# Performance work log

Hardware: AMD Instinct MI355X
Metric: run time of the kernel (lower is better)

The kernel has to match this reference:

```python
import jax, jax.numpy as jnp
import numpy as np

B, S, DIM, NH = 2, 2048, 1536, 12
HD = DIM // NH            # 128
C = HD // 2               # 64 rotary pairs
CF = C - 2 * (C // 3)     # 22 (frame axis)
CH = C // 3               # 21 (height axis)
CW = C // 3               # 21 (width axis)
GF, GH, GW = 8, 16, 16    # grid sizes, GF*GH*GW == S
EPS = 1e-6


def _freq_table(n_pos, dim):
    inv = 1.0 / (10000.0 ** (np.arange(dim, dtype=np.float64) / dim))
    ang = np.outer(np.arange(n_pos, dtype=np.float64), inv)
    return (np.cos(ang).astype(np.float32), np.sin(ang).astype(np.float32))


def setup_inputs() -> dict:
    key = jax.random.key(0)
    ks = jax.random.split(key, 8)
    scale = 0.02
    cos_f, sin_f = _freq_table(GF, CF)
    cos_h, sin_h = _freq_table(GH, CH)
    cos_w, sin_w = _freq_table(GW, CW)
    return {
        'x': jax.random.normal(ks[0], (B, S, DIM), dtype=jnp.float32),
        'seq_lens': jnp.array([2048, 1600], dtype=jnp.int32),
        'f': GF, 'h': GH, 'w': GW,
        'wq': scale * jax.random.normal(ks[1], (DIM, DIM), dtype=jnp.float32),
        'bq': jnp.zeros((DIM,), jnp.float32),
        'wk': scale * jax.random.normal(ks[2], (DIM, DIM), dtype=jnp.float32),
        'bk': jnp.zeros((DIM,), jnp.float32),
        'wv': scale * jax.random.normal(ks[3], (DIM, DIM), dtype=jnp.float32),
        'bv': jnp.zeros((DIM,), jnp.float32),
        'wo': scale * jax.random.normal(ks[4], (DIM, DIM), dtype=jnp.float32),
        'bo': jnp.zeros((DIM,), jnp.float32),
        'nq_w': jnp.ones((DIM,), jnp.float32),
        'nk_w': jnp.ones((DIM,), jnp.float32),
        'cos_f': jnp.asarray(cos_f), 'sin_f': jnp.asarray(sin_f),
        'cos_h': jnp.asarray(cos_h), 'sin_h': jnp.asarray(sin_h),
        'cos_w': jnp.asarray(cos_w), 'sin_w': jnp.asarray(sin_w),
    }


def _rmsnorm(t, wt):
    return t * jax.lax.rsqrt(jnp.mean(t * t, axis=-1, keepdims=True) + EPS) * wt


def _grid_rope(t, cos, sin, b, s):
    # t: [b, s, NH, HD] ; cos/sin: [s, 1, C] (per-position assembled freqs)
    tp = t.reshape(b, s, NH, C, 2)
    xr, xi = tp[..., 0], tp[..., 1]
    rr = xr * cos - xi * sin          # complex multiply by e^{i*theta}
    ri = xr * sin + xi * cos
    return jnp.stack([rr, ri], axis=-1).reshape(b, s, NH, HD)


def reference(x, seq_lens, f, h, w, wq, bq, wk, bk, wv, bv, wo, bo,
              nq_w, nk_w, cos_f, sin_f, cos_h, sin_h, cos_w, sin_w):
    b, s, _ = x.shape
    # QKV projections with RMSNorm on q/k over full dim (as in the module)
    q = _rmsnorm(x @ wq.T + bq, nq_w).reshape(b, s, NH, HD)
    k = _rmsnorm(x @ wk.T + bk, nk_w).reshape(b, s, NH, HD)
    v = (x @ wv.T + bv).reshape(b, s, NH, HD)
    # grid-indexed RoPE: zero offsets / target==grid => arange sampling per axis
    idx = jnp.arange(s)
    fi = idx // (h * w)
    hi = (idx // w) % h
    wi = idx % w
    cos = jnp.concatenate([cos_f[fi], cos_h[hi], cos_w[wi]], axis=-1)[:, None, :]
    sin = jnp.concatenate([sin_f[fi], sin_h[hi], sin_w[wi]], axis=-1)[:, None, :]
    qr = _grid_rope(q, cos, sin, b, s)
    kr = _grid_rope(k, cos, sin, b, s)
    # attention with ragged key-length masking (flash_attention k_lens)
    scale = 1.0 / jnp.sqrt(jnp.float32(HD))
    scores = jnp.einsum('bqnd,bknd->bnqk', qr, kr) * scale
    kmask = idx[None, :] < seq_lens[:, None]            # [b, s]
    scores = jnp.where(kmask[:, None, None, :], scores, jnp.float32(-1e30))
    attn = jax.nn.softmax(scores, axis=-1)
    out = jnp.einsum('bnqk,bknd->bqnd', attn, v).reshape(b, s, DIM)
    return out @ wo.T + bo
```

## Files before the change

kernel.cpp:

```cpp
#include <hip/hip_runtime.h>
#include <hip/hip_bf16.h>
#include <math.h>

#define DIM_  1536
#define NH_   12
#define HD_   128
#define S_    2048
#define B_    2
#define M_    (B_*S_)

typedef __attribute__((ext_vector_type(8))) _Float16 f16x8;
typedef __attribute__((ext_vector_type(4))) short short4v;
typedef __attribute__((ext_vector_type(8))) short short8v;
typedef __attribute__((ext_vector_type(4))) float f32x4;

#define SSCALE_LOG2E (0.08838834764831845f * 1.4426950408889634f)

static __device__ __forceinline__ short f2h(float f) {
  union { _Float16 h; short s; } u;
  u.h = (_Float16)f;
  return u.s;
}

static __device__ __forceinline__ unsigned pk2h(float a, float b) {
  typedef __attribute__((ext_vector_type(2))) __fp16 fp16x2;
  union { fp16x2 v; unsigned u; } u2;
  u2.v = __builtin_amdgcn_cvt_pkrtz(a, b);
  return u2.u;
}

__global__ __launch_bounds__(256) void f2h_k(
    const float* __restrict__ in, short* __restrict__ out, int n8)
{
  int i = blockIdx.x * 256 + threadIdx.x;
  if (i >= n8) return;
  const float4* p = (const float4*)in + (size_t)i * 2;
  float4 a = p[0], b = p[1];
  short8v o;
  o[0] = f2h(a.x); o[1] = f2h(a.y); o[2] = f2h(a.z); o[3] = f2h(a.w);
  o[4] = f2h(b.x); o[5] = f2h(b.y); o[6] = f2h(b.z); o[7] = f2h(b.w);
  *((short8v*)out + i) = o;
}

static __device__ __forceinline__ void gemm128_core(
    const short* __restrict__ A16, const float* __restrict__ W,
    const float* __restrict__ bias, float* __restrict__ Out,
    int m0, int n0)
{
  __shared__ __align__(16) char Atile[8192];
  __shared__ __align__(16) char Btile[8192];
  const int tid = threadIdx.x;
  const int l  = tid & 63, w = tid >> 6;
  const int wr = w >> 1, wc = w & 1;
  const int lc = l & 15, lg = l >> 4;

  f32x4 acc[4][4] = {};

  for (int k0 = 0; k0 < DIM_; k0 += 32) {
#pragma unroll
    for (int i = 0; i < 2; ++i) {
      int row   = i * 64 + w * 16 + (l >> 2);
      int slot  = l & 3;
      int gslot = slot ^ ((row >> 1) & 3);
      const short* g = A16 + (size_t)(m0 + row) * DIM_ + k0 + gslot * 8;
      __builtin_amdgcn_global_load_lds(
          (const __attribute__((address_space(1))) unsigned*)g,
          (__attribute__((address_space(3))) unsigned*)(Atile + i * 4096 + w * 1024),
          16, 0, 0);
    }
#pragma unroll
    for (int i = 0; i < 4; ++i) {
      int e   = tid + i * 256;
      int row = e >> 3, f4 = e & 7;
      float4 v4 = *(const float4*)(W + (size_t)(n0 + row) * DIM_ + k0 + f4 * 4);
      short4v h4;
      h4[0] = f2h(v4.x); h4[1] = f2h(v4.y); h4[2] = f2h(v4.z); h4[3] = f2h(v4.w);
      int slot = f4 >> 1;
      *(short4v*)(Btile + row * 64 + (((slot ^ ((row >> 1) & 3)) << 4)) + ((f4 & 1) << 3)) = h4;
    }
    __syncthreads();

    f16x8 af[4], bf[4];
#pragma unroll
    for (int mt = 0; mt < 4; ++mt) {
      int ar = wr * 64 + mt * 16 + lc;
      af[mt] = *(const f16x8*)(Atile + ar * 64 + ((lg ^ ((ar >> 1) & 3)) << 4));
    }
#pragma unroll
    for (int nt = 0; nt < 4; ++nt) {
      int br = wc * 64 + nt * 16 + lc;
      bf[nt] = *(const f16x8*)(Btile + br * 64 + ((lg ^ ((br >> 1) & 3)) << 4));
    }
#pragma unroll
    for (int mt = 0; mt < 4; ++mt)
#pragma unroll
      for (int nt = 0; nt < 4; ++nt)
        acc[mt][nt] = __builtin_amdgcn_mfma_f32_16x16x32_f16(af[mt], bf[nt], acc[mt][nt], 0, 0, 0);
    __syncthreads();
  }

#pragma unroll
  for (int nt = 0; nt < 4; ++nt) {
    int col = n0 + wc * 64 + nt * 16 + lc;
    float bb = bias[col];
#pragma unroll
    for (int mt = 0; mt < 4; ++mt) {
#pragma unroll
      for (int r = 0; r < 4; ++r) {
        int rowm = m0 + wr * 64 + mt * 16 + lg * 4 + r;
        Out[(size_t)rowm * DIM_ + col] = acc[mt][nt][r] + bb;
      }
    }
  }
}

__global__ __launch_bounds__(256) void gemm_qkv_k(
    const short* __restrict__ x16,
    const float* __restrict__ wq, const float* __restrict__ wk, const float* __restrict__ wv,
    const float* __restrict__ bq, const float* __restrict__ bk, const float* __restrict__ bv,
    float* __restrict__ qf, float* __restrict__ kf, float* __restrict__ vf)
{
  const int z = blockIdx.z;
  const float* W  = (z == 0) ? wq : (z == 1) ? wk : wv;
  const float* bi = (z == 0) ? bq : (z == 1) ? bk : bv;
  float*       O  = (z == 0) ? qf : (z == 1) ? kf : vf;
  gemm128_core(x16, W, bi, O, blockIdx.y * 128, blockIdx.x * 128);
}

__global__ __launch_bounds__(256) void gemm_out_k(
    const short* __restrict__ att16, const float* __restrict__ wo,
    const float* __restrict__ bo, float* __restrict__ out)
{
  gemm128_core(att16, wo, bo, out, blockIdx.y * 128, blockIdx.x * 128);
}

__global__ __launch_bounds__(256) void rms_rope_pack_k(
    const float* __restrict__ t, const float* __restrict__ w,
    const float* __restrict__ cf, const float* __restrict__ sf,
    const float* __restrict__ ch, const float* __restrict__ sh,
    const float* __restrict__ cw, const float* __restrict__ sw,
    short* __restrict__ outb, float qsc)
{
  const int row = blockIdx.x;
  const int b   = row >> 11;
  const int s   = row & (S_ - 1);
  const float* rp = t + (size_t)row * DIM_;

  float ss = 0.f;
  for (int i = threadIdx.x; i < DIM_; i += 256) { float v2 = rp[i]; ss += v2 * v2; }
#pragma unroll
  for (int off = 32; off > 0; off >>= 1) ss += __shfl_down(ss, off);
  __shared__ float red[4];
  if ((threadIdx.x & 63) == 0) red[threadIdx.x >> 6] = ss;
  __syncthreads();
  float scale = rsqrtf((red[0] + red[1] + red[2] + red[3]) * (1.f / DIM_) + 1e-6f) * qsc;

  const int fi = s >> 8;
  const int hi = (s >> 4) & 15;
  const int wi = s & 15;

  for (int p = threadIdx.x; p < NH_ * 64; p += 256) {
    int n = p >> 6, c = p & 63;
    float co, si;
    if (c < 22)      { co = cf[fi * 22 + c];        si = sf[fi * 22 + c]; }
    else if (c < 43) { co = ch[hi * 21 + (c - 22)]; si = sh[hi * 21 + (c - 22)]; }
    else             { co = cw[wi * 21 + (c - 43)]; si = sw[wi * 21 + (c - 43)]; }
    int d0 = n * HD_ + 2 * c;
    float xr = rp[d0]     * scale * w[d0];
    float xi = rp[d0 + 1] * scale * w[d0 + 1];
    float rr = xr * co - xi * si;
    float ri = xr * si + xi * co;
    *(unsigned int*)(outb + (((size_t)(b * NH_ + n) * S_ + s) * HD_ + 2 * c)) = pk2h(rr, ri);
  }
}

__global__ __launch_bounds__(256) void v_transpose_k(
    const float* __restrict__ v, short* __restrict__ vtb)
{
  const int bh = blockIdx.y;
  const int b  = bh / NH_;
  const int h  = bh - b * NH_;
  const int s0 = blockIdx.x << 6;
  __shared__ short tile[64][130];
  const int tid = threadIdx.x;
#pragma unroll
  for (int i = 0; i < 8; ++i) {
    int f  = tid + (i << 8);
    int sl = f >> 5, d4 = f & 31;
    float4 t4 = *(const float4*)(v + (size_t)(b * S_ + s0 + sl) * DIM_ + h * 128 + d4 * 4);
    tile[sl][d4 * 4 + 0] = f2h(t4.x);
    tile[sl][d4 * 4 + 1] = f2h(t4.y);
    tile[sl][d4 * 4 + 2] = f2h(t4.z);
    tile[sl][d4 * 4 + 3] = f2h(t4.w);
  }
  __syncthreads();
#pragma unroll
  for (int i = 0; i < 8; ++i) {
    int f  = tid + (i << 8);
    int d  = f >> 4, s4 = f & 15;
    short4v o4;
    o4[0] = tile[s4 * 4 + 0][d];
    o4[1] = tile[s4 * 4 + 1][d];
    o4[2] = tile[s4 * 4 + 2][d];
    o4[3] = tile[s4 * 4 + 3][d];
    *(short4v*)(vtb + ((size_t)bh * HD_ + d) * S_ + s0 + s4 * 4) = o4;
  }
}

__global__ __launch_bounds__(256) void attn_mfma5_k(
    const short* __restrict__ qb, const short* __restrict__ kb,
    const short* __restrict__ vtb, const int* __restrict__ seq_lens,
    short* __restrict__ o16)
{
  const int bh = blockIdx.y;
  const int b  = bh / NH_;
  const int h  = bh - b * NH_;
  const int q0 = blockIdx.x << 6;
  const int kvlen = seq_lens[b];
  const int tid  = threadIdx.x;
  const int wid  = tid >> 6;
  const int lane = tid & 63;
  const int lg   = lane >> 4;
  const int lc   = lane & 15;
  const int xo   = (lc & 7) << 4;

  __shared__ __align__(16) char Kt[16384];
  __shared__ __align__(16) char Vt[16384];
  __shared__ __align__(16) char Pt[4][2048];

  f16x8 bq[4];
  {
    const size_t base = ((size_t)bh * S_ + q0 + wid * 16 + lc) * HD_;
#pragma unroll
    for (int dc = 0; dc < 4; ++dc)
      bq[dc] = *(const f16x8*)(qb + base + dc * 32 + lg * 8);
  }

  const short* kgA = kb + ((size_t)bh * S_ + wid * 16 + lg) * HD_
                        + ((lc * 8) ^ (lg << 3));
  const short* kgB = kb + ((size_t)bh * S_ + wid * 16 + 4 + lg) * HD_
                        + ((lc * 8) ^ ((lg ^ 4) << 3));
  const short* vg  = vtb + ((size_t)bh * HD_ + wid * 32 + (lane >> 3)) * S_
                         + (((lane & 7) * 8) ^ ((lane >> 3) << 3));

#define STAGE_K()                                                              \
  {                                                                            \
    _Pragma("unroll")                                                          \
    for (int j = 0; j < 4; ++j) {                                              \
      const short* g = (j & 1) ? (kgB + ((j - 1) >> 1) * (8 * HD_))            \
                               : (kgA + (j >> 1) * (8 * HD_));                 \
      __builtin_amdgcn_global_load_lds(                                        \
          (const __attribute__((address_space(1))) unsigned*)g,                \
          (__attribute__((address_space(3))) unsigned*)(Kt + (wid * 16 + j * 4) * 256), \
          16, 0, 0);                                                           \
    }                                                                          \
  }
#define STAGE_V()                                                              \
  {                                                                            \
    _Pragma("unroll")                                                          \
    for (int j = 0; j < 4; ++j) {                                              \
      __builtin_amdgcn_global_load_lds(                                        \
          (const __attribute__((address_space(1))) unsigned*)(vg + j * 8 * S_),\
          (__attribute__((address_space(3))) unsigned*)(Vt + (wid * 32 + j * 8) * 128), \
          16, 0, 0);                                                           \
    }                                                                          \
  }

  f32x4 oacc[8] = {};
  float m = -3.0e38f, l = 0.f;

  const int nt = kvlen >> 6;

  STAGE_K();
  kgA += 64 * HD_; kgB += 64 * HD_;
  __syncthreads();

  for (int ti = 0; ti < nt; ++ti) {
    STAGE_V();
    vg += 64;

    f32x4 s[4];
    __builtin_amdgcn_s_setprio(1);
#pragma unroll
    for (int kt = 0; kt < 4; ++kt) {
      f32x4 a = {0.f, 0.f, 0.f, 0.f};
      const char* kr = Kt + (kt * 16 + lc) * 256;
#pragma unroll
      for (int dc = 0; dc < 4; ++dc) {
        f16x8 kf = *(const f16x8*)(kr + ((dc * 64 + lg * 16) ^ xo));
        a = __builtin_amdgcn_mfma_f32_16x16x32_f16(kf, bq[dc], a, 0, 0, 0);
      }
      s[kt] = a;
    }
    __builtin_amdgcn_s_setprio(0);

    float t0 = -3.0e38f;
#pragma unroll
    for (int kt = 0; kt < 4; ++kt)
#pragma unroll
      for (int r = 0; r < 4; ++r) t0 = fmaxf(t0, s[kt][r]);
    t0 = fmaxf(t0, __shfl_xor(t0, 16));
    t0 = fmaxf(t0, __shfl_xor(t0, 32));

    if (__any(t0 > m + 8.f)) {
      float mn = fmaxf(m, t0);
      float a  = exp2f(m - mn);
      m = mn; l *= a;
#pragma unroll
      for (int r = 0; r < 4; ++r) {
        float ar = __shfl(a, 4 * lg + r);
#pragma unroll
        for (int n = 0; n < 8; ++n) oacc[n][r] *= ar;
      }
    }
    float ls = 0.f;
#pragma unroll
    for (int kt = 0; kt < 4; ++kt)
#pragma unroll
      for (int r = 0; r < 4; ++r) {
        float p = exp2f(s[kt][r] - m); s[kt][r] = p; ls += p;
      }
    ls += __shfl_xor(ls, 16);
    ls += __shfl_xor(ls, 32);
    l += ls;

    {
      char* pr = Pt[wid] + lc * 128;
#pragma unroll
      for (int kt = 0; kt < 4; ++kt) {
#pragma unroll
        for (int rr = 0; rr < 2; ++rr) {
          unsigned u = pk2h(s[kt][2 * rr], s[kt][2 * rr + 1]);
          int off = (kt * 32 + lg * 8 + rr * 4) ^ xo;
          *(unsigned*)(pr + off) = u;
        }
      }
    }

    __syncthreads();

    if (ti + 1 < nt) {
      STAGE_K();
      kgA += 64 * HD_; kgB += 64 * HD_;
    }

    __builtin_amdgcn_s_setprio(1);
#pragma unroll
    for (int kc = 0; kc < 2; ++kc) {
      f16x8 pa = *(const f16x8*)(Pt[wid] + lc * 128 + ((kc * 64 + lg * 16) ^ xo));
#pragma unroll
      for (int n = 0; n < 8; ++n) {
        f16x8 vf = *(const f16x8*)(Vt + (n * 16 + lc) * 128 + ((kc * 64 + lg * 16) ^ xo));
        oacc[n] = __builtin_amdgcn_mfma_f32_16x16x32_f16(pa, vf, oacc[n], 0, 0, 0);
      }
    }
    __builtin_amdgcn_s_setprio(0);

    __syncthreads();
  }

#pragma unroll
  for (int r = 0; r < 4; ++r) {
    float li = 1.f / __shfl(l, 4 * lg + r);
    int qrow = q0 + wid * 16 + 4 * lg + r;
#pragma unroll
    for (int n = 0; n < 8; ++n)
      o16[((size_t)(b * S_ + qrow) * NH_ + h) * HD_ + n * 16 + lc] = f2h(oacc[n][r] * li);
  }
#undef STAGE_K
#undef STAGE_V
}

extern "C" void kernel_launch(void* const* d_in, const int* in_sizes, int n_in,
                              void* d_out, int out_size, void* d_ws, size_t ws_size,
                              hipStream_t stream) {
  const float* x        = (const float*)d_in[0];
  const int*   seq_lens = (const int*)d_in[1];
  const float* wq = (const float*)d_in[5];
  const float* bq = (const float*)d_in[6];
  const float* wk = (const float*)d_in[7];
  const float* bk = (const float*)d_in[8];
  const float* wv = (const float*)d_in[9];
  const float* bv = (const float*)d_in[10];
  const float* wo = (const float*)d_in[11];
  const float* bo = (const float*)d_in[12];
  const float* nq = (const float*)d_in[13];
  const float* nk = (const float*)d_in[14];
  const float* cf = (const float*)d_in[15];
  const float* sf = (const float*)d_in[16];
  const float* ch = (const float*)d_in[17];
  const float* sh = (const float*)d_in[18];
  const float* cw = (const float*)d_in[19];
  const float* sw = (const float*)d_in[20];

  const size_t rowelems = (size_t)M_ * DIM_;
  float* qf  = (float*)d_ws;
  float* kf  = qf + rowelems;
  float* vf  = kf + rowelems;
  short* x16 = (short*)(vf + rowelems);
  short* vt  = x16;
  short* qh  = (short*)vf;
  short* kh  = qh + rowelems;
  short* att16 = (short*)qf;
  float* out = (float*)d_out;

  f2h_k<<<(int)(rowelems / 8 / 256), 256, 0, stream>>>(x, x16, (int)(rowelems / 8));

  gemm_qkv_k<<<dim3(DIM_ / 128, M_ / 128, 3), 256, 0, stream>>>(
      x16, wq, wk, wv, bq, bk, bv, qf, kf, vf);

  v_transpose_k<<<dim3(S_ / 64, B_ * NH_), 256, 0, stream>>>(vf, vt);

  rms_rope_pack_k<<<M_, 256, 0, stream>>>(qf, nq, cf, sf, ch, sh, cw, sw, qh,
                                          SSCALE_LOG2E);
  rms_rope_pack_k<<<M_, 256, 0, stream>>>(kf, nk, cf, sf, ch, sh, cw, sw, kh, 1.0f);

  attn_mfma5_k<<<dim3(S_ / 64, B_ * NH_), 256, 0, stream>>>(qh, kh, vt, seq_lens, att16);

  gemm_out_k<<<dim3(DIM_ / 128, M_ / 128), 256, 0, stream>>>(att16, wo, bo, out);
}
```

Baseline: 269.0 us.

## Pre-convert weights to fp16 and load both GEMM operands directly into LDS

Weights are converted to fp16 once per call in a fused conversion kernel instead of being converted per tile inside every GEMM block. Both GEMM operands are then streamed straight into shared memory with direct global-to-LDS loads. The V projection writes fp16 output, so the transpose kernel reads half the bytes and uses wider vectors. This adds extra conversion launches and workspace for the fp16 weights, and changes how workspace buffers are aliased.

```diff
diff --git a/kernel.cpp b/kernel.cpp
--- a/kernel.cpp
+++ b/kernel.cpp
@@ -8,6 +8,7 @@
 #define S_    2048
 #define B_    2
 #define M_    (B_*S_)
+#define WEL_  (DIM_*DIM_)
 
 typedef __attribute__((ext_vector_type(8))) _Float16 f16x8;
 typedef __attribute__((ext_vector_type(4))) short short4v;
@@ -42,9 +43,29 @@
   *((short8v*)out + i) = o;
 }
 
-static __device__ __forceinline__ void gemm128_core(
-    const short* __restrict__ A16, const float* __restrict__ W,
-    const float* __restrict__ bias, float* __restrict__ Out,
+__global__ __launch_bounds__(256) void f2h4_k(
+    const float* __restrict__ x, const float* __restrict__ wq,
+    const float* __restrict__ wk, const float* __restrict__ wv,
+    short* __restrict__ x16, short* __restrict__ w16)
+{
+  int i = blockIdx.x * 256 + threadIdx.x;
+  const float* src; short* dst; int j;
+  if (i < 786432)       { src = x;  dst = x16;            j = i; }
+  else if (i < 1081344) { src = wq; dst = w16;            j = i - 786432; }
+  else if (i < 1376256) { src = wk; dst = w16 + WEL_;     j = i - 1081344; }
+  else                  { src = wv; dst = w16 + 2 * WEL_; j = i - 1376256; }
+  const float4* p = (const float4*)src + (size_t)j * 2;
+  float4 a = p[0], b = p[1];
+  short8v o;
+  o[0] = f2h(a.x); o[1] = f2h(a.y); o[2] = f2h(a.z); o[3] = f2h(a.w);
+  o[4] = f2h(b.x); o[5] = f2h(b.y); o[6] = f2h(b.z); o[7] = f2h(b.w);
+  *((short8v*)dst + j) = o;
+}
+
+template<bool F16OUT>
+static __device__ __forceinline__ void gemm16_core(
+    const short* __restrict__ A16, const short* __restrict__ W16,
+    const float* __restrict__ bias, void* __restrict__ Outp,
     int m0, int n0)
 {
   __shared__ __align__(16) char Atile[8192];
@@ -56,28 +77,26 @@
 
   f32x4 acc[4][4] = {};
 
+  const int rs  = w * 16 + (l >> 2);
+  const int gsl = ((l & 3) ^ ((rs >> 1) & 3)) * 8;
+  const short* gA0 = A16 + (size_t)(m0 + rs) * DIM_ + gsl;
+  const short* gA1 = A16 + (size_t)(m0 + 64 + rs) * DIM_ + gsl;
+  const short* gB0 = W16 + (size_t)(n0 + rs) * DIM_ + gsl;
+  const short* gB1 = W16 + (size_t)(n0 + 64 + rs) * DIM_ + gsl;
+
   for (int k0 = 0; k0 < DIM_; k0 += 32) {
-#pragma unroll
-    for (int i = 0; i < 2; ++i) {
-      int row   = i * 64 + w * 16 + (l >> 2);
-      int slot  = l & 3;
-      int gslot = slot ^ ((row >> 1) & 3);
-      const short* g = A16 + (size_t)(m0 + row) * DIM_ + k0 + gslot * 8;
-      __builtin_amdgcn_global_load_lds(
-          (const __attribute__((address_space(1))) unsigned*)g,
-          (__attribute__((address_space(3))) unsigned*)(Atile + i * 4096 + w * 1024),
-          16, 0, 0);
-    }
-#pragma unroll
-    for (int i = 0; i < 4; ++i) {
-      int e   = tid + i * 256;
-      int row = e >> 3, f4 = e & 7;
-      float4 v4 = *(const float4*)(W + (size_t)(n0 + row) * DIM_ + k0 + f4 * 4);
-      short4v h4;
-      h4[0] = f2h(v4.x); h4[1] = f2h(v4.y); h4[2] = f2h(v4.z); h4[3] = f2h(v4.w);
-      int slot = f4 >> 1;
-      *(short4v*)(Btile + row * 64 + (((slot ^ ((row >> 1) & 3)) << 4)) + ((f4 & 1) << 3)) = h4;
-    }
+    __builtin_amdgcn_global_load_lds(
+        (const __attribute__((address_space(1))) unsigned*)(gA0 + k0),
+        (__attribute__((address_space(3))) unsigned*)(Atile + w * 1024), 16, 0, 0);
+    __builtin_amdgcn_global_load_lds(
+        (const __attribute__((address_space(1))) unsigned*)(gA1 + k0),
+        (__attribute__((address_space(3))) unsigned*)(Atile + 4096 + w * 1024), 16, 0, 0);
+    __builtin_amdgcn_global_load_lds(
+        (const __attribute__((address_space(1))) unsigned*)(gB0 + k0),
+        (__attribute__((address_space(3))) unsigned*)(Btile + w * 1024), 16, 0, 0);
+    __builtin_amdgcn_global_load_lds(
+        (const __attribute__((address_space(1))) unsigned*)(gB1 + k0),
+        (__attribute__((address_space(3))) unsigned*)(Btile + 4096 + w * 1024), 16, 0, 0);
     __syncthreads();
 
     f16x8 af[4], bf[4];
@@ -108,30 +127,38 @@
 #pragma unroll
       for (int r = 0; r < 4; ++r) {
         int rowm = m0 + wr * 64 + mt * 16 + lg * 4 + r;
-        Out[(size_t)rowm * DIM_ + col] = acc[mt][nt][r] + bb;
-      }
-    }
-  }
-}
-
-__global__ __launch_bounds__(256) void gemm_qkv_k(
-    const short* __restrict__ x16,
-    const float* __restrict__ wq, const float* __restrict__ wk, const float* __restrict__ wv,
-    const float* __restrict__ bq, const float* __restrict__ bk, const float* __restrict__ bv,
-    float* __restrict__ qf, float* __restrict__ kf, float* __restrict__ vf)
+        if (F16OUT)
+          ((short*)Outp)[(size_t)rowm * DIM_ + col] = f2h(acc[mt][nt][r] + bb);
+        else
+          ((float*)Outp)[(size_t)rowm * DIM_ + col] = acc[mt][nt][r] + bb;
+      }
+    }
+  }
+}
+
+__global__ __launch_bounds__(256) void gemm_qk_k(
+    const short* __restrict__ x16, const short* __restrict__ w16,
+    const float* __restrict__ bq, const float* __restrict__ bk,
+    float* __restrict__ qf, float* __restrict__ kf)
 {
   const int z = blockIdx.z;
-  const float* W  = (z == 0) ? wq : (z == 1) ? wk : wv;
-  const float* bi = (z == 0) ? bq : (z == 1) ? bk : bv;
-  float*       O  = (z == 0) ? qf : (z == 1) ? kf : vf;
-  gemm128_core(x16, W, bi, O, blockIdx.y * 128, blockIdx.x * 128);
-}
-
-__global__ __launch_bounds__(256) void gemm_out_k(
-    const short* __restrict__ att16, const float* __restrict__ wo,
+  gemm16_core<false>(x16, w16 + (size_t)z * WEL_, z ? bk : bq,
+                     z ? (void*)kf : (void*)qf,
+                     blockIdx.y * 128, blockIdx.x * 128);
+}
+
+__global__ __launch_bounds__(256) void gemm_v16_k(
+    const short* __restrict__ x16, const short* __restrict__ wv16,
+    const float* __restrict__ bv, short* __restrict__ vf16)
+{
+  gemm16_core<true>(x16, wv16, bv, vf16, blockIdx.y * 128, blockIdx.x * 128);
+}
+
+__global__ __launch_bounds__(256) void gemm_out16_k(
+    const short* __restrict__ att16, const short* __restrict__ wo16,
     const float* __restrict__ bo, float* __restrict__ out)
 {
-  gemm128_core(att16, wo, bo, out, blockIdx.y * 128, blockIdx.x * 128);
+  gemm16_core<false>(att16, wo16, bo, out, blockIdx.y * 128, blockIdx.x * 128);
 }
 
 __global__ __launch_bounds__(256) void rms_rope_pack_k(
@@ -174,36 +201,32 @@
   }
 }
 
-__global__ __launch_bounds__(256) void v_transpose_k(
-    const float* __restrict__ v, short* __restrict__ vtb)
+__global__ __launch_bounds__(256) void v_transpose16_k(
+    const short* __restrict__ v16, short* __restrict__ vtb)
 {
   const int bh = blockIdx.y;
   const int b  = bh / NH_;
   const int h  = bh - b * NH_;
   const int s0 = blockIdx.x << 6;
-  __shared__ short tile[64][130];
+  __shared__ short tile[64][136];
   const int tid = threadIdx.x;
 #pragma unroll
-  for (int i = 0; i < 8; ++i) {
+  for (int i = 0; i < 4; ++i) {
     int f  = tid + (i << 8);
-    int sl = f >> 5, d4 = f & 31;
-    float4 t4 = *(const float4*)(v + (size_t)(b * S_ + s0 + sl) * DIM_ + h * 128 + d4 * 4);
-    tile[sl][d4 * 4 + 0] = f2h(t4.x);
-    tile[sl][d4 * 4 + 1] = f2h(t4.y);
-    tile[sl][d4 * 4 + 2] = f2h(t4.z);
-    tile[sl][d4 * 4 + 3] = f2h(t4.w);
+    int sl = f >> 4, d8 = f & 15;
+    short8v v8 = *(const short8v*)(v16 + (size_t)(b * S_ + s0 + sl) * DIM_ + h * 128 + d8 * 8);
+#pragma unroll
+    for (int j = 0; j < 8; ++j) tile[sl][d8 * 8 + j] = v8[j];
   }
   __syncthreads();
 #pragma unroll
-  for (int i = 0; i < 8; ++i) {
+  for (int i = 0; i < 4; ++i) {
     int f  = tid + (i << 8);
-    int d  = f >> 4, s4 = f & 15;
-    short4v o4;
-    o4[0] = tile[s4 * 4 + 0][d];
-    o4[1] = tile[s4 * 4 + 1][d];
-    o4[2] = tile[s4 * 4 + 2][d];
-    o4[3] = tile[s4 * 4 + 3][d];
-    *(short4v*)(vtb + ((size_t)bh * HD_ + d) * S_ + s0 + s4 * 4) = o4;
+    int d  = f >> 3, s8 = f & 7;
+    short8v o8;
+#pragma unroll
+    for (int j = 0; j < 8; ++j) o8[j] = tile[s8 * 8 + j][d];
+    *(short8v*)(vtb + ((size_t)bh * HD_ + d) * S_ + s0 + s8 * 8) = o8;
   }
 }
 
@@ -394,28 +417,34 @@
   const float* sw = (const float*)d_in[20];
 
   const size_t rowelems = (size_t)M_ * DIM_;
-  float* qf  = (float*)d_ws;
-  float* kf  = qf + rowelems;
-  float* vf  = kf + rowelems;
-  short* x16 = (short*)(vf + rowelems);
-  short* vt  = x16;
-  short* qh  = (short*)vf;
-  short* kh  = qh + rowelems;
-  short* att16 = (short*)qf;
-  float* out = (float*)d_out;
-
-  f2h_k<<<(int)(rowelems / 8 / 256), 256, 0, stream>>>(x, x16, (int)(rowelems / 8));
-
-  gemm_qkv_k<<<dim3(DIM_ / 128, M_ / 128, 3), 256, 0, stream>>>(
-      x16, wq, wk, wv, bq, bk, bv, qf, kf, vf);
-
-  v_transpose_k<<<dim3(S_ / 64, B_ * NH_), 256, 0, stream>>>(vf, vt);
+  float* qf   = (float*)d_ws;
+  float* kf   = qf + rowelems;
+  short* vf16 = (short*)(kf + rowelems);
+  short* x16  = vf16 + rowelems;
+  short* w16  = x16 + rowelems;
+  short* vt   = x16;
+  short* qh   = vf16;
+  short* kh   = (short*)d_ws + rowelems;
+  short* att16 = (short*)d_ws;
+  short* wo16 = (short*)kf;
+  float* out  = (float*)d_out;
+
+  f2h4_k<<<6528, 256, 0, stream>>>(x, wq, wk, wv, x16, w16);
+
+  gemm_qk_k<<<dim3(DIM_ / 128, M_ / 128, 2), 256, 0, stream>>>(
+      x16, w16, bq, bk, qf, kf);
+  gemm_v16_k<<<dim3(DIM_ / 128, M_ / 128), 256, 0, stream>>>(
+      x16, w16 + 2 * (size_t)WEL_, bv, vf16);
+
+  v_transpose16_k<<<dim3(S_ / 64, B_ * NH_), 256, 0, stream>>>(vf16, vt);
 
   rms_rope_pack_k<<<M_, 256, 0, stream>>>(qf, nq, cf, sf, ch, sh, cw, sw, qh,
                                           SSCALE_LOG2E);
   rms_rope_pack_k<<<M_, 256, 0, stream>>>(kf, nk, cf, sf, ch, sh, cw, sw, kh, 1.0f);
 
+  f2h_k<<<1152, 256, 0, stream>>>(wo, wo16, WEL_ / 8);
+
   attn_mfma5_k<<<dim3(S_ / 64, B_ * NH_), 256, 0, stream>>>(qh, kh, vt, seq_lens, att16);
 
-  gemm_out_k<<<dim3(DIM_ / 128, M_ / 128), 256, 0, stream>>>(att16, wo, bo, out);
-}
+  gemm_out16_k<<<dim3(DIM_ / 128, M_ / 128), 256, 0, stream>>>(att16, wo16, bo, out);
+}
```

Measured after the change: 254.0 us. 5.6% less time.
